# Kernel tuning notes

Hardware: AMD Instinct MI355X
Metric: run time of the kernel (lower is better)

The kernel has to match this reference:

```python
import jax, jax.numpy as jnp
import numpy as np

B, H, W, C = 32, 56, 56, 256
WS, SHIFT, HEADS = 7, 3, 8
HD = C // HEADS
HIDDEN = 4 * C
N = WS * WS
NW = (H // WS) * (W // WS)
EPS = 1e-5


def _rel_pos_indices():
    coords = np.stack(np.meshgrid(np.arange(WS), np.arange(WS), indexing='ij'), -1).reshape(-1, 2)
    rel = coords[None, :, :] - coords[:, None, :]
    rel[..., 0] += WS - 1
    rel[..., 1] += WS - 1
    rel[..., 0] *= 2 * WS - 1
    return rel.sum(-1)  # (N, N) int

_REL_IDX = jnp.asarray(_rel_pos_indices())


def _attn_mask():
    img = np.zeros((H, W), np.float32)
    sl = (slice(0, -WS), slice(-WS, -SHIFT), slice(-SHIFT, None))
    tag = 0
    for hs in sl:
        for ws_ in sl:
            img[hs, ws_] = tag
            tag += 1
    mw = img.reshape(H // WS, WS, W // WS, WS).transpose(0, 2, 1, 3).reshape(-1, N)
    diff = mw[:, None, :] - mw[:, :, None]
    return jnp.asarray(np.where(diff != 0, -100.0, 0.0).astype(np.float32))  # (NW, N, N)

_MASK = _attn_mask()


def _layernorm(x, g, b):
    mu = x.mean(-1, keepdims=True)
    var = ((x - mu) ** 2).mean(-1, keepdims=True)
    return (x - mu) * jax.lax.rsqrt(var + EPS) * g + b


def _win_partition(x):  # (B,H,W,C) -> (B*NW, N, C)
    x = x.reshape(B, H // WS, WS, W // WS, WS, C)
    return x.transpose(0, 1, 3, 2, 4, 5).reshape(-1, N, C)


def _win_reverse(w):  # (B*NW, N, C) -> (B,H,W,C)
    x = w.reshape(B, H // WS, W // WS, WS, WS, C)
    return x.transpose(0, 1, 3, 2, 4, 5).reshape(B, H, W, C)


def setup_inputs() -> dict:
    key = jax.random.key(0)
    ks = jax.random.split(key, 16)
    s = 0.02
    return {
        'x': jax.random.normal(ks[0], (B, H * W, C), jnp.float32),
        'norm1_g': jnp.ones((C,), jnp.float32),
        'norm1_b': jnp.zeros((C,), jnp.float32),
        'qkv_w': jax.random.normal(ks[1], (C, 3 * C), jnp.float32) * s,
        'qkv_b': jnp.zeros((3 * C,), jnp.float32),
        'rel_bias': jax.random.normal(ks[2], ((2 * WS - 1) ** 2, HEADS), jnp.float32) * s,
        'proj_w': jax.random.normal(ks[3], (C, C), jnp.float32) * s,
        'proj_b': jnp.zeros((C,), jnp.float32),
        'norm2_g': jnp.ones((C,), jnp.float32),
        'norm2_b': jnp.zeros((C,), jnp.float32),
        'fc1_w': jax.random.normal(ks[4], (C, HIDDEN), jnp.float32) * s,
        'fc1_b': jnp.zeros((HIDDEN,), jnp.float32),
        'fc2_w': jax.random.normal(ks[5], (HIDDEN, C), jnp.float32) * s,
        'fc2_b': jnp.zeros((C,), jnp.float32),
    }


def reference(x, norm1_g, norm1_b, qkv_w, qkv_b, rel_bias, proj_w, proj_b,
              norm2_g, norm2_b, fc1_w, fc1_b, fc2_w, fc2_b):
    shortcut = x
    h = _layernorm(x, norm1_g, norm1_b).reshape(B, H, W, C)
    h = jnp.roll(h, (-SHIFT, -SHIFT), axis=(1, 2))
    xw = _win_partition(h)  # (B*NW, N, C)

    qkv = xw @ qkv_w + qkv_b  # (B*NW, N, 3C)
    qkv = qkv.reshape(-1, N, 3, HEADS, HD).transpose(2, 0, 3, 1, 4)
    q, k, v = qkv[0], qkv[1], qkv[2]  # (B*NW, HEADS, N, HD)
    q = q * (HD ** -0.5)
    attn = jnp.einsum('whnd,whmd->whnm', q, k)  # (B*NW, HEADS, N, N)

    bias = rel_bias[_REL_IDX].transpose(2, 0, 1)  # (HEADS, N, N)
    attn = attn + bias[None]
    attn = attn.reshape(B, NW, HEADS, N, N) + _MASK[None, :, None]
    attn = jax.nn.softmax(attn.reshape(-1, HEADS, N, N), axis=-1)

    out = jnp.einsum('whnm,whmd->whnd', attn, v)  # (B*NW, HEADS, N, HD)
    out = out.transpose(0, 2, 1, 3).reshape(-1, N, C)
    out = out @ proj_w + proj_b

    h = _win_reverse(out)
    h = jnp.roll(h, (SHIFT, SHIFT), axis=(1, 2)).reshape(B, H * W, C)

    x = shortcut + h
    m = _layernorm(x, norm2_g, norm2_b)
    m = jax.nn.gelu(m @ fc1_w + fc1_b, approximate=False) @ fc2_w + fc2_b
    return x + m
```

## Files before the change

### kernel.cpp

```cpp
#include <hip/hip_runtime.h>
#include <math.h>

static constexpr long T_TOK = 100352;

typedef __attribute__((ext_vector_type(8))) short short8;
typedef __attribute__((ext_vector_type(8))) unsigned short ushort8v;
typedef __attribute__((ext_vector_type(4))) float floatx4;

__device__ __forceinline__ float b2f(unsigned short u) {
    return __uint_as_float(((unsigned)u) << 16);
}
__device__ __forceinline__ unsigned short f2b(float f) {
    unsigned u = __float_as_uint(f);
    u += 0x7FFFu + ((u >> 16) & 1u);
    return (unsigned short)(u >> 16);
}

__device__ __forceinline__ void gload_lds16(const unsigned short* g, unsigned short* l) {
    __builtin_amdgcn_global_load_lds(
        (const __attribute__((address_space(1))) void*)g,
        (__attribute__((address_space(3))) void*)l, 16, 0, 0);
}

__global__ void detect_kernel(const unsigned short* __restrict__ x, int* flag) {
    __shared__ int cnt;
    if (threadIdx.x == 0) cnt = 0;
    __syncthreads();
    int local = 0;
    for (int i = 0; i < 16; ++i) {
        float a = fabsf(b2f(x[threadIdx.x * 16 + i]));
        if (a >= 0.015625f && a <= 8.0f) local++;
    }
    atomicAdd(&cnt, local);
    __syncthreads();
    if (threadIdx.x == 0) *flag = (cnt < 3072) ? 1 : 0;
}

__global__ void conv_kernel(const void* __restrict__ src, unsigned short* __restrict__ dst,
                            int n, const int* __restrict__ flag) {
    int i = blockIdx.x * 256 + threadIdx.x;
    if (i >= n) return;
    if (*flag) dst[i] = f2b(((const float*)src)[i]);
    else       dst[i] = ((const unsigned short*)src)[i];
}

__global__ void convT_kernel(const void* __restrict__ src, unsigned short* __restrict__ dst,
                             int K, int N, const int* __restrict__ flag) {
    int i = blockIdx.x * 256 + threadIdx.x;
    if (i >= K * N) return;
    int k = i / N, n = i - k * N;
    unsigned short v = (*flag) ? f2b(((const float*)src)[i])
                               : ((const unsigned short*)src)[i];
    dst[(long)n * K + k] = v;
}

__global__ __launch_bounds__(256) void ln_kernel(
    const void* __restrict__ xin,
    const unsigned short* __restrict__ g,
    const unsigned short* __restrict__ bsh,
    unsigned short* __restrict__ out, int mode, const int* __restrict__ flagp)
{
    int lane = threadIdx.x & 63;
    int wv = threadIdx.x >> 6;
    long t = (long)blockIdx.x * 4 + wv;
    int c0 = lane * 4;
    bool f32 = flagp && (*flagp != 0);
    float v0, v1, v2, v3;
    if (f32) {
        float4 xv = *(const float4*)((const float*)xin + t * 256 + c0);
        v0 = xv.x; v1 = xv.y; v2 = xv.z; v3 = xv.w;
    } else {
        ushort4 xv = *(const ushort4*)((const unsigned short*)xin + t * 256 + c0);
        v0 = b2f(xv.x); v1 = b2f(xv.y); v2 = b2f(xv.z); v3 = b2f(xv.w);
    }
    float s1 = v0 + v1 + v2 + v3;
    float s2 = v0*v0 + v1*v1 + v2*v2 + v3*v3;
    #pragma unroll
    for (int off = 32; off > 0; off >>= 1) {
        s1 += __shfl_down(s1, off, 64);
        s2 += __shfl_down(s2, off, 64);
    }
    s1 = __shfl(s1, 0, 64);
    s2 = __shfl(s2, 0, 64);
    float mean = s1 * (1.0f / 256.0f);
    float var  = s2 * (1.0f / 256.0f) - mean * mean;
    float rs = rsqrtf(fmaxf(var, 0.0f) + 1e-5f);
    ushort4 gv = *(const ushort4*)(g + c0);
    ushort4 bv = *(const ushort4*)(bsh + c0);
    ushort4 ov;
    ov.x = f2b((v0 - mean) * rs * b2f(gv.x) + b2f(bv.x));
    ov.y = f2b((v1 - mean) * rs * b2f(gv.y) + b2f(bv.y));
    ov.z = f2b((v2 - mean) * rs * b2f(gv.z) + b2f(bv.z));
    ov.w = f2b((v3 - mean) * rs * b2f(gv.w) + b2f(bv.w));
    long oidx;
    if (mode == 0) {
        int b_ = (int)(t / 3136);
        int hw = (int)(t % 3136);
        int hh = hw / 56, wc = hw % 56;
        int i = hh - 3; if (i < 0) i += 56;
        int j = wc - 3; if (j < 0) j += 56;
        oidx = ((long)(b_ * 64 + (i / 7) * 8 + (j / 7)) * 49
                + (i % 7) * 7 + (j % 7)) * 256 + c0;
    } else {
        oidx = t * 256 + c0;
    }
    *(ushort4*)(out + oidx) = ov;
}

__global__ __launch_bounds__(256) void gemm_mfma(
    const unsigned short* __restrict__ A,
    const unsigned short* __restrict__ Bt,
    const unsigned short* __restrict__ bias,
    void* __restrict__ out,
    const void* __restrict__ res,
    int M, int N, int K, int mode,
    const int* __restrict__ resflag, const int* __restrict__ oflag)
{
    __shared__ __align__(16) unsigned short lds[2][8192];
    const int tid  = threadIdx.x;
    const int lane = tid & 63, wave = tid >> 6;
    const int q = lane >> 4, l16 = lane & 15;
    const int wm = wave >> 1, wn = wave & 1;

    const int gx  = (int)gridDim.x;
    const int nwg = gx * (int)gridDim.y;
    const int lin = (int)blockIdx.y * gx + (int)blockIdx.x;
    const int chunk = nwg >> 3;
    const int lin2 = (lin & 7) * chunk + (lin >> 3);
    const int bx = lin2 % gx, by = lin2 / gx;

    const long m0 = (long)by * 128;
    const int  n0 = bx * 128;

    const int srow  = tid >> 2;
    const int skcol = (tid & 3) * 8;

    floatx4 acc[4][4];
    #pragma unroll
    for (int i = 0; i < 4; ++i)
        #pragma unroll
        for (int j = 0; j < 4; ++j)
            acc[i][j] = (floatx4){0.f, 0.f, 0.f, 0.f};

    const unsigned short* Ag = A  + (m0 + srow) * (long)K + skcol;
    const unsigned short* Bg = Bt + ((long)(n0 + srow)) * K + skcol;
    const long rowK64 = 64 * (long)K;
    const int  wbase  = wave * 512;

#define STAGE(b, t) do {                                       \
        const int k0_ = (t) << 5;                              \
        unsigned short* Lb = &lds[(b)][wbase];                 \
        gload_lds16(Ag + k0_,          Lb);                    \
        gload_lds16(Ag + k0_ + rowK64, Lb + 2048);             \
        gload_lds16(Bg + k0_,          Lb + 4096);             \
        gload_lds16(Bg + k0_ + rowK64, Lb + 6144);             \
    } while (0)
#define SBAR() do {                                            \
        __builtin_amdgcn_sched_barrier(0);                     \
        __builtin_amdgcn_s_barrier();                          \
        __builtin_amdgcn_sched_barrier(0);                     \
    } while (0)

    const int nt = K >> 5;
    STAGE(0, 0);
    STAGE(1, 1);
    int cur = 0;
    for (int t = 0; t < nt; ++t) {
        if (t + 1 < nt) asm volatile("s_waitcnt vmcnt(4)" ::: "memory");
        else            asm volatile("s_waitcnt vmcnt(0)" ::: "memory");
        SBAR();
        short8 af[4], bfr[4];
        #pragma unroll
        for (int i = 0; i < 4; ++i)
            af[i] = *(const short8*)&lds[cur][(wm * 64 + i * 16 + l16) * 32 + q * 8];
        #pragma unroll
        for (int j = 0; j < 4; ++j)
            bfr[j] = *(const short8*)&lds[cur][4096 + (wn * 64 + j * 16 + l16) * 32 + q * 8];
        #pragma unroll
        for (int i = 0; i < 4; ++i)
            #pragma unroll
            for (int j = 0; j < 4; ++j)
                acc[i][j] = __builtin_amdgcn_mfma_f32_16x16x32_bf16(
                    af[i], bfr[j], acc[i][j], 0, 0, 0);
        SBAR();
        if (t + 2 < nt) STAGE(cur, t + 2);
        cur ^= 1;
    }
#undef STAGE
#undef SBAR

    const bool resf32 = resflag && (*resflag != 0);
    const bool outf32 = oflag && (*oflag != 0);
    unsigned short* outb = (unsigned short*)out;
    float* outf = (float*)out;
    #pragma unroll
    for (int i = 0; i < 4; ++i) {
        #pragma unroll
        for (int r = 0; r < 4; ++r) {
            long grow = m0 + wm * 64 + i * 16 + q * 4 + r;
            long natRow = 0;
            if (mode == 1) {
                int w = (int)(grow / 49), n = (int)(grow % 49);
                int b_ = w >> 6, widx = w & 63;
                int wi = widx >> 3, wj = widx & 7;
                int pi = n / 7, pj = n % 7;
                int ii = wi * 7 + pi, jj = wj * 7 + pj;
                int h = ii + 3; if (h >= 56) h -= 56;
                int wc = jj + 3; if (wc >= 56) wc -= 56;
                natRow = ((long)b_ * 3136 + h * 56 + wc);
            }
            #pragma unroll
            for (int j = 0; j < 4; ++j) {
                int gcol = n0 + wn * 64 + j * 16 + l16;
                float v = acc[i][j][r] + b2f(bias[gcol]);
                if (mode == 2) {
                    v = 0.5f * v * (1.0f + erff(v * 0.70710678118654752f));
                    outb[grow * N + gcol] = f2b(v);
                } else if (mode == 0) {
                    outb[grow * N + gcol] = f2b(v);
                } else if (mode == 3) {
                    long o = grow * N + gcol;
                    float rv = outf32 ? outf[o] : b2f(((const unsigned short*)res)[o]);
                    v += rv;
                    if (outf32) outf[o] = v; else outb[o] = f2b(v);
                } else {
                    long o = natRow * 256 + gcol;
                    float rv = resf32 ? ((const float*)res)[o]
                                      : b2f(((const unsigned short*)res)[o]);
                    v += rv;
                    if (outf32) outf[o] = v; else outb[o] = f2b(v);
                }
            }
        }
    }
}

__global__ __launch_bounds__(256) void attn_mfma(
    const unsigned short* __restrict__ qkv,
    const unsigned short* __restrict__ rel_bias,
    unsigned short* __restrict__ out)
{
    __shared__ __align__(16) unsigned short bias_s[1360];
    __shared__ __align__(16) unsigned short Vt[4][32][72];
    __shared__ __align__(16) unsigned short Ps[4][64][72];
    const int tid = threadIdx.x;
    const int lane = tid & 63, wave = tid >> 6;
    const int q = lane >> 4, l16 = lane & 15;
    const int unit = blockIdx.x * 4 + wave;
    const int w = unit >> 3, h = unit & 7;
    const int widx = w & 63, wi = widx >> 3, wj = widx & 7;

    for (int e = tid; e < 1352; e += 256) bias_s[e] = rel_bias[e];

    const long vbase = (long)w * 49 * 768 + 512 + h * 32;
    #pragma unroll 4
    for (int it = 0; it < 32; ++it) {
        int idx = it * 64 + lane;
        int key = idx >> 5, d = idx & 31;
        unsigned short v = (key < 49) ? qkv[vbase + (long)key * 768 + d]
                                      : (unsigned short)0;
        Vt[wave][d][key] = v;
    }
    __syncthreads();

    const long qbase = (long)w * 49 * 768 + h * 32;
    short8 qf[4], kf[4];
    #pragma unroll
    for (int i = 0; i < 4; ++i) {
        int qr = l16 + 16 * i; if (qr > 48) qr = 48;
        qf[i] = *(const short8*)(qkv + qbase + (long)qr * 768 + q * 8);
    }
    #pragma unroll
    for (int j = 0; j < 4; ++j) {
        int kr = l16 + 16 * j; if (kr > 48) kr = 48;
        kf[j] = *(const short8*)(qkv + qbase + 256 + (long)kr * 768 + q * 8);
    }

    floatx4 sc[4][4];
    #pragma unroll
    for (int i = 0; i < 4; ++i)
        #pragma unroll
        for (int j = 0; j < 4; ++j)
            sc[i][j] = __builtin_amdgcn_mfma_f32_16x16x32_bf16(
                qf[i], kf[j], (floatx4){0.f, 0.f, 0.f, 0.f}, 0, 0, 0);

    int imj[4], jmj[4], tmj[4], validj[4];
    #pragma unroll
    for (int j = 0; j < 4; ++j) {
        int key = 16 * j + l16;
        validj[j] = key < 49;
        int k2 = validj[j] ? key : 48;
        int im = k2 / 7, jm = k2 - im * 7;
        imj[j] = im; jmj[j] = jm;
        int rm = wi * 7 + im, cm = wj * 7 + jm;
        tmj[j] = (rm < 49 ? 0 : (rm < 53 ? 1 : 2)) * 3
               + (cm < 49 ? 0 : (cm < 53 ? 1 : 2));
    }

    const float scale = 0.17677669529663687f;
    #pragma unroll
    for (int i = 0; i < 4; ++i) {
        #pragma unroll
        for (int r = 0; r < 4; ++r) {
            int query = 16 * i + 4 * q + r;
            int qn = query > 48 ? 48 : query;
            int in_ = qn / 7, jn = qn - in_ * 7;
            int rn = wi * 7 + in_, cn = wj * 7 + jn;
            int tn = (rn < 49 ? 0 : (rn < 53 ? 1 : 2)) * 3
                   + (cn < 49 ? 0 : (cn < 53 ? 1 : 2));
            float sv[4];
            float mx = -1e30f;
            #pragma unroll
            for (int j = 0; j < 4; ++j) {
                float s = sc[i][j][r] * scale;
                int ridx = (imj[j] - in_ + 6) * 13 + (jmj[j] - jn + 6);
                s += b2f(bias_s[ridx * 8 + h]);
                if (tmj[j] != tn) s -= 100.0f;
                if (!validj[j]) s = -1e30f;
                sv[j] = s;
                mx = fmaxf(mx, s);
            }
            #pragma unroll
            for (int m = 1; m < 16; m <<= 1)
                mx = fmaxf(mx, __shfl_xor(mx, m, 64));
            float sum = 0.0f;
            #pragma unroll
            for (int j = 0; j < 4; ++j) { sv[j] = __expf(sv[j] - mx); sum += sv[j]; }
            #pragma unroll
            for (int m = 1; m < 16; m <<= 1)
                sum += __shfl_xor(sum, m, 64);
            float inv = 1.0f / sum;
            #pragma unroll
            for (int j = 0; j < 4; ++j)
                Ps[wave][query][16 * j + l16] = f2b(sv[j] * inv);
        }
    }

    floatx4 oacc[4][2];
    #pragma unroll
    for (int i = 0; i < 4; ++i)
        #pragma unroll
        for (int jd = 0; jd < 2; ++jd)
            oacc[i][jd] = (floatx4){0.f, 0.f, 0.f, 0.f};
    #pragma unroll
    for (int s = 0; s < 2; ++s) {
        short8 vfr[2];
        #pragma unroll
        for (int jd = 0; jd < 2; ++jd)
            vfr[jd] = *(const short8*)&Vt[wave][l16 + 16 * jd][32 * s + q * 8];
        #pragma unroll
        for (int i = 0; i < 4; ++i) {
            short8 pfr = *(const short8*)&Ps[wave][l16 + 16 * i][32 * s + q * 8];
            #pragma unroll
            for (int jd = 0; jd < 2; ++jd)
                oacc[i][jd] = __builtin_amdgcn_mfma_f32_16x16x32_bf16(
                    pfr, vfr[jd], oacc[i][jd], 0, 0, 0);
        }
    }

    const long obase = (long)w * 49 * 256 + h * 32;
    #pragma unroll
    for (int i = 0; i < 4; ++i) {
        #pragma unroll
        for (int r = 0; r < 4; ++r) {
            int query = 16 * i + 4 * q + r;
            if (query < 49) {
                #pragma unroll
                for (int jd = 0; jd < 2; ++jd)
                    out[obase + (long)query * 256 + 16 * jd + l16] =
                        f2b(oacc[i][jd][r]);
            }
        }
    }
}

extern "C" void kernel_launch(void* const* d_in, const int* in_sizes, int n_in,
                              void* d_out, int out_size, void* d_ws, size_t ws_size,
                              hipStream_t stream) {
    (void)n_in; (void)out_size; (void)ws_size; (void)in_sizes;
    unsigned short* ws  = (unsigned short*)d_ws;
    const size_t TT = (size_t)T_TOK;

    unsigned short* r0  = ws;
    unsigned short* r1  = ws + TT * 256;
    unsigned short* pb  = ws + TT * 256 + TT * 1024;
    const size_t O_QKVW = 0,      O_QKVB = 196608, O_RELB = 197376, O_PROJW = 198728;
    const size_t O_PROJB = 264264, O_N1G = 264520, O_N1B = 264776;
    const size_t O_N2G = 265032,  O_N2B = 265288, O_FC1W = 265544, O_FC1B = 527688;
    const size_t O_FC2W = 528712, O_FC2B = 790856, O_PEND = 791112;
    int* flag = (int*)(pb + O_PEND);

    detect_kernel<<<1, 256, 0, stream>>>((const unsigned short*)d_in[0], flag);

    struct { int idx; size_t off; int n; } cv[9] = {
        {1, O_N1G, 256}, {2, O_N1B, 256}, {4, O_QKVB, 768},
        {5, O_RELB, 1352}, {7, O_PROJB, 256},
        {8, O_N2G, 256}, {9, O_N2B, 256}, {11, O_FC1B, 1024}, {13, O_FC2B, 256},
    };
    for (int i = 0; i < 9; ++i)
        conv_kernel<<<(cv[i].n + 255) / 256, 256, 0, stream>>>(
            d_in[cv[i].idx], pb + cv[i].off, cv[i].n, flag);
    convT_kernel<<<(196608 + 255) / 256, 256, 0, stream>>>(d_in[3],  pb + O_QKVW, 256, 768,  flag);
    convT_kernel<<<(65536  + 255) / 256, 256, 0, stream>>>(d_in[6],  pb + O_PROJW, 256, 256, flag);
    convT_kernel<<<(262144 + 255) / 256, 256, 0, stream>>>(d_in[10], pb + O_FC1W, 256, 1024, flag);
    convT_kernel<<<(262144 + 255) / 256, 256, 0, stream>>>(d_in[12], pb + O_FC2W, 1024, 256, flag);

    const long T = T_TOK;
    unsigned short* xw       = r0;
    unsigned short* qkv      = r1;
    unsigned short* attn_out = r0;
    unsigned short* x2n      = r0;
    unsigned short* hidden   = r1;

    ln_kernel<<<dim3(T / 4), 256, 0, stream>>>(d_in[0], pb + O_N1G, pb + O_N1B, xw, 0, flag);
    gemm_mfma<<<dim3(6, T / 128), 256, 0, stream>>>(xw, pb + O_QKVW, pb + O_QKVB, qkv,
                                                    nullptr, (int)T, 768, 256, 0,
                                                    nullptr, nullptr);
    attn_mfma<<<dim3(4096), 256, 0, stream>>>(qkv, pb + O_RELB, attn_out);
    gemm_mfma<<<dim3(2, T / 128), 256, 0, stream>>>(attn_out, pb + O_PROJW, pb + O_PROJB,
                                                    d_out, d_in[0], (int)T, 256, 256, 1,
                                                    flag, flag);
    ln_kernel<<<dim3(T / 4), 256, 0, stream>>>(d_out, pb + O_N2G, pb + O_N2B, x2n, 1, flag);
    gemm_mfma<<<dim3(8, T / 128), 256, 0, stream>>>(x2n, pb + O_FC1W, pb + O_FC1B, hidden,
                                                    nullptr, (int)T, 1024, 256, 2,
                                                    nullptr, nullptr);
    gemm_mfma<<<dim3(2, T / 128), 256, 0, stream>>>(hidden, pb + O_FC2W, pb + O_FC2B, d_out,
                                                    d_out, (int)T, 256, 1024, 3,
                                                    nullptr, flag);
}
```

Measured before the change: 985.5 us.

## Fuse MLP fc1, GELU and fc2 into one kernel keeping hidden in LDS

Replaces the two MLP GEMM launches with one kernel. Each 32-row block computes fc1 plus exact GELU into an 80KB LDS hidden tile, then runs fc2 with the residual add. This removes the global-memory round trip of the 1024-wide hidden activation. In exchange, weights are read straight from global memory without LDS staging and are re-read by every 32-row block, and the large LDS footprint limits occupancy.

```diff
diff --git a/kernel.cpp b/kernel.cpp
--- a/kernel.cpp
+++ b/kernel.cpp
@@ -235,6 +235,129 @@
     }
 }
 
+__global__ __launch_bounds__(256) void mlp_fused(
+    const unsigned short* __restrict__ X,
+    const unsigned short* __restrict__ W1t,
+    const unsigned short* __restrict__ B1,
+    const unsigned short* __restrict__ W2t,
+    const unsigned short* __restrict__ B2,
+    void* __restrict__ out,
+    const int* __restrict__ oflag)
+{
+    __shared__ __align__(16) unsigned short Xs[32 * 256];
+    __shared__ __align__(16) unsigned short Hs[32 * 1024];
+    const int tid = threadIdx.x;
+    const int lane = tid & 63, wave = tid >> 6;
+    const int q = lane >> 4, l16 = lane & 15;
+    const long m0 = (long)blockIdx.x * 32;
+
+    #pragma unroll
+    for (int t = 0; t < 4; ++t) {
+        int s = t * 256 + tid;
+        int row = s >> 5, colS = (s & 31) * 8;
+        int colG = colS ^ ((row & 7) << 3);
+        gload_lds16(X + (m0 + row) * 256 + colG,
+                    Xs + t * 2048 + wave * 512);
+    }
+    __syncthreads();
+
+    #pragma unroll 1
+    for (int c = 0; c < 4; ++c) {
+        floatx4 acc[2][4];
+        #pragma unroll
+        for (int i = 0; i < 2; ++i)
+            #pragma unroll
+            for (int j = 0; j < 4; ++j)
+                acc[i][j] = (floatx4){0.f, 0.f, 0.f, 0.f};
+        #pragma unroll
+        for (int ks = 0; ks < 8; ++ks) {
+            const int k0 = ks * 32;
+            short8 af[2], bfr[4];
+            #pragma unroll
+            for (int i = 0; i < 2; ++i) {
+                int row = i * 16 + l16;
+                int col = (k0 + q * 8) ^ ((row & 7) << 3);
+                af[i] = *(const short8*)&Xs[row * 256 + col];
+            }
+            #pragma unroll
+            for (int j = 0; j < 4; ++j) {
+                int n = c * 256 + wave * 64 + j * 16 + l16;
+                bfr[j] = *(const short8*)(W1t + (long)n * 256 + k0 + q * 8);
+            }
+            #pragma unroll
+            for (int i = 0; i < 2; ++i)
+                #pragma unroll
+                for (int j = 0; j < 4; ++j)
+                    acc[i][j] = __builtin_amdgcn_mfma_f32_16x16x32_bf16(
+                        af[i], bfr[j], acc[i][j], 0, 0, 0);
+        }
+        #pragma unroll
+        for (int i = 0; i < 2; ++i) {
+            #pragma unroll
+            for (int r = 0; r < 4; ++r) {
+                int row = i * 16 + q * 4 + r;
+                int sw = (row & 7) << 3;
+                #pragma unroll
+                for (int j = 0; j < 4; ++j) {
+                    int col = c * 256 + wave * 64 + j * 16 + l16;
+                    float v = acc[i][j][r] + b2f(B1[col]);
+                    v = 0.5f * v * (1.0f + erff(v * 0.70710678118654752f));
+                    Hs[row * 1024 + (col ^ sw)] = f2b(v);
+                }
+            }
+        }
+    }
+    __syncthreads();
+
+    floatx4 acc2[2][4];
+    #pragma unroll
+    for (int i = 0; i < 2; ++i)
+        #pragma unroll
+        for (int j = 0; j < 4; ++j)
+            acc2[i][j] = (floatx4){0.f, 0.f, 0.f, 0.f};
+    #pragma unroll 8
+    for (int ks = 0; ks < 32; ++ks) {
+        const int k0 = ks * 32;
+        short8 af[2], bfr[4];
+        #pragma unroll
+        for (int i = 0; i < 2; ++i) {
+            int row = i * 16 + l16;
+            int col = (k0 + q * 8) ^ ((row & 7) << 3);
+            af[i] = *(const short8*)&Hs[row * 1024 + col];
+        }
+        #pragma unroll
+        for (int j = 0; j < 4; ++j) {
+            int n = wave * 64 + j * 16 + l16;
+            bfr[j] = *(const short8*)(W2t + (long)n * 1024 + k0 + q * 8);
+        }
+        #pragma unroll
+        for (int i = 0; i < 2; ++i)
+            #pragma unroll
+            for (int j = 0; j < 4; ++j)
+                acc2[i][j] = __builtin_amdgcn_mfma_f32_16x16x32_bf16(
+                    af[i], bfr[j], acc2[i][j], 0, 0, 0);
+    }
+    const bool outf32 = oflag && (*oflag != 0);
+    unsigned short* outb = (unsigned short*)out;
+    float* outf = (float*)out;
+    #pragma unroll
+    for (int i = 0; i < 2; ++i) {
+        #pragma unroll
+        for (int r = 0; r < 4; ++r) {
+            long grow = m0 + i * 16 + q * 4 + r;
+            #pragma unroll
+            for (int j = 0; j < 4; ++j) {
+                int gcol = wave * 64 + j * 16 + l16;
+                long o = grow * 256 + gcol;
+                float v = acc2[i][j][r] + b2f(B2[gcol]);
+                float rv = outf32 ? outf[o] : b2f(outb[o]);
+                v += rv;
+                if (outf32) outf[o] = v; else outb[o] = f2b(v);
+            }
+        }
+    }
+}
+
 __global__ __launch_bounds__(256) void attn_mfma(
     const unsigned short* __restrict__ qkv,
     const unsigned short* __restrict__ rel_bias,
@@ -410,7 +533,6 @@
     unsigned short* qkv      = r1;
     unsigned short* attn_out = r0;
     unsigned short* x2n      = r0;
-    unsigned short* hidden   = r1;
 
     ln_kernel<<<dim3(T / 4), 256, 0, stream>>>(d_in[0], pb + O_N1G, pb + O_N1B, xw, 0, flag);
     gemm_mfma<<<dim3(6, T / 128), 256, 0, stream>>>(xw, pb + O_QKVW, pb + O_QKVB, qkv,
@@ -421,10 +543,6 @@
                                                     d_out, d_in[0], (int)T, 256, 256, 1,
                                                     flag, flag);
     ln_kernel<<<dim3(T / 4), 256, 0, stream>>>(d_out, pb + O_N2G, pb + O_N2B, x2n, 1, flag);
-    gemm_mfma<<<dim3(8, T / 128), 256, 0, stream>>>(x2n, pb + O_FC1W, pb + O_FC1B, hidden,
-                                                    nullptr, (int)T, 1024, 256, 2,
-                                                    nullptr, nullptr);
-    gemm_mfma<<<dim3(2, T / 128), 256, 0, stream>>>(hidden, pb + O_FC2W, pb + O_FC2B, d_out,
-                                                    d_out, (int)T, 256, 1024, 3,
-                                                    nullptr, flag);
-}
+    mlp_fused<<<dim3(T / 32), 256, 0, stream>>>(x2n, pb + O_FC1W, pb + O_FC1B,
+                                                pb + O_FC2W, pb + O_FC2B, d_out, flag);
+}
```

Measured after the change: 1.143 ms. 16.0% more time.
